# Kernel tuning notes

Measured on AMD Instinct MI355X. Metric: run time of the kernel, lower is better.

The kernel has to match this reference:

```python
import jax, jax.numpy as jnp
import numpy as np

N, E, B, O = 100000, 1600000, 256, 32
D, H, OD = 128, 128, 32  # node_features, hidden_dim, order_encoding_dim
L = 3  # num_layers


def setup_inputs() -> dict:
    key = jax.random.key(0)
    ks = jax.random.split(key, 32)
    g = lambda k, s, fan: jax.random.normal(k, s, jnp.float32) * (1.0 / np.sqrt(fan))
    inp = {
        'x': jax.random.normal(ks[0], (N, D), jnp.float32),
        'edge_index': jax.random.randint(ks[1], (2, E), 0, N),
        'orders': jax.random.normal(ks[2], (B, O, OD), jnp.float32),
        'batch': jnp.sort(jax.random.randint(ks[3], (N,), 0, B)),
        # GIN layers (input_dim == hidden_dim so all 3 layers stack): MLP = Lin(H,H)->ReLU->Lin(H,H), then BatchNorm1d
        'gW1': g(ks[4], (L, H, H), H), 'gb1': jnp.zeros((L, H)),
        'gW2': g(ks[5], (L, H, H), H), 'gb2': jnp.zeros((L, H)),
        'gamma': jnp.ones((L, H)), 'beta': jnp.zeros((L, H)),
        # order encoder: Lin(OD,H)->ReLU->Lin(H,H)
        'oW1': g(ks[6], (OD, H), OD), 'ob1': jnp.zeros((H,)),
        'oW2': g(ks[7], (H, H), H), 'ob2': jnp.zeros((H,)),
        # score head: Lin(4H,H)->ReLU->Lin(H,H//2)->ReLU->Lin(H//2,1)
        'sW1': g(ks[8], (4 * H, H), 4 * H), 'sb1': jnp.zeros((H,)),
        'sW2': g(ks[9], (H, H // 2), H), 'sb2': jnp.zeros((H // 2,)),
        'sW3': g(ks[10], (H // 2, 1), H // 2), 'sb3': jnp.zeros((1,)),
    }
    return inp


def reference(x, edge_index, orders, batch, gW1, gb1, gW2, gb2, gamma, beta,
              oW1, ob1, oW2, ob2, sW1, sb1, sW2, sb2, sW3, sb3):
    n = x.shape[0]
    src, dst = edge_index[0], edge_index[1]
    h = x
    nl = gW1.shape[0]
    for i in range(nl):  # fixed small layer count
        agg = jax.ops.segment_sum(h[src], dst, num_segments=n)  # sum aggregation
        z = agg + h  # (1 + eps) * x with eps = 0 (GINConv default)
        z = jnp.maximum(z @ gW1[i] + gb1[i], 0) @ gW2[i] + gb2[i]
        mu = z.mean(0)
        var = z.var(0)  # biased var, as torch BN uses for normalization
        z = (z - mu) * jax.lax.rsqrt(var + 1e-5) * gamma[i] + beta[i]
        h = jnp.maximum(z, 0) if i < nl - 1 else z  # dropout inactive (eval)
    b = orders.shape[0]
    cnt = jax.ops.segment_sum(jnp.ones((n,), h.dtype), batch, num_segments=b)
    ssum = jax.ops.segment_sum(h, batch, num_segments=b)
    smean = ssum / jnp.maximum(cnt, 1)[:, None]
    smax = jax.ops.segment_max(h, batch, num_segments=b)
    smax = jnp.where(jnp.isfinite(smax), smax, 0)
    graph = jnp.concatenate([smean, smax, ssum], axis=-1)  # [B, 3H]
    # batched over num_orders (equivalent to the python per-order loop)
    oe = jnp.maximum(orders @ oW1 + ob1, 0) @ oW2 + ob2  # [B, O, H]
    comb = jnp.concatenate(
        [jnp.broadcast_to(graph[:, None, :], (b, orders.shape[1], graph.shape[-1])), oe], axis=-1)
    s = jnp.maximum(comb @ sW1 + sb1, 0)
    s = jnp.maximum(s @ sW2 + sb2, 0)
    s = (s @ sW3 + sb3)[..., 0]  # [B, O]
    return s
```

## Files before the change

### kernel.cpp

```cpp
#include <hip/hip_runtime.h>

static constexpr int NN = 100000;
static constexpr int NE = 1600000;
static constexpr int NB = 256;
static constexpr int NO = 32;
static constexpr int HD = 128;
static constexpr long NH = (long)NN * HD;

static constexpr int BSHIFT = 9;
static constexpr int BSIZE = 1 << BSHIFT;
static constexpr int NBUCK = 256;
static constexpr int CHUNK = 16384;
static constexpr int NCHUNK = (NE + CHUNK - 1) / CHUNK;
static constexpr int POOL_ROWS = 64;
static constexpr int POOL_GRID = (NN + POOL_ROWS - 1) / POOL_ROWS;

typedef _Float16 f16x8 __attribute__((ext_vector_type(8)));
typedef _Float16 f16x4 __attribute__((ext_vector_type(4)));
typedef _Float16 f16x2 __attribute__((ext_vector_type(2)));
typedef float f32x4 __attribute__((ext_vector_type(4)));

__device__ __forceinline__ unsigned int encf(float f) {
  unsigned int u = __float_as_uint(f);
  return (u & 0x80000000u) ? ~u : (u | 0x80000000u);
}
__device__ __forceinline__ float decf(unsigned int e) {
  return (e & 0x80000000u) ? __uint_as_float(e & 0x7fffffffu) : __uint_as_float(~e);
}

__global__ void bucket_count(const int* __restrict__ ei, int* __restrict__ bucketTotal) {
  __shared__ int cnt[NBUCK];
  const int t = threadIdx.x;
  cnt[t] = 0;
  __syncthreads();
  long start = (long)blockIdx.x * CHUNK;
  long end = min((long)NE, start + CHUNK);
  for (long e = start + t; e < end; e += 256)
    atomicAdd(&cnt[ei[NE + e] >> BSHIFT], 1);
  __syncthreads();
  if (cnt[t]) atomicAdd(&bucketTotal[t], cnt[t]);
}

__global__ void bucket_scan(const int* __restrict__ bucketTotal, int* __restrict__ bucketBase,
                            int* __restrict__ cursor) {
  __shared__ int part[NBUCK];
  const int t = threadIdx.x;
  int v = bucketTotal[t];
  part[t] = v;
  __syncthreads();
  for (int off = 1; off < NBUCK; off <<= 1) {
    int u = (t >= off) ? part[t - off] : 0;
    __syncthreads();
    part[t] += u;
    __syncthreads();
  }
  int base = part[t] - v;
  bucketBase[t] = base;
  cursor[t] = base;
  if (t == NBUCK - 1) bucketBase[NBUCK] = part[t];
}

__global__ void bucket_scatter(const int* __restrict__ ei, int* __restrict__ cursor,
                               unsigned int* __restrict__ binned) {
  __shared__ int cnt[NBUCK];
  __shared__ int runbase[NBUCK];
  const int t = threadIdx.x;
  cnt[t] = 0;
  __syncthreads();
  long start = (long)blockIdx.x * CHUNK;
  long end = min((long)NE, start + CHUNK);
  for (long e = start + t; e < end; e += 256)
    atomicAdd(&cnt[ei[NE + e] >> BSHIFT], 1);
  __syncthreads();
  int c = cnt[t];
  runbase[t] = c ? atomicAdd(&cursor[t], c) : 0;
  cnt[t] = 0;
  __syncthreads();
  for (long e = start + t; e < end; e += 256) {
    int d = ei[NE + e], s = ei[e];
    int b = d >> BSHIFT;
    int pos = runbase[b] + atomicAdd(&cnt[b], 1);
    binned[pos] = ((unsigned int)s << BSHIFT) | (unsigned int)(d & (BSIZE - 1));
  }
}

__global__ void bucket_csr(const unsigned int* __restrict__ binned,
                           const int* __restrict__ bucketBase,
                           int* __restrict__ rowptr, int* __restrict__ col) {
  __shared__ int cnt[BSIZE];
  __shared__ int excl[BSIZE];
  __shared__ int cur[BSIZE];
  __shared__ int part[256];
  const int b = blockIdx.x;
  const int t = threadIdx.x;
  const int lo = bucketBase[b], hi = bucketBase[b + 1];
  cnt[t] = 0; cnt[t + 256] = 0;
  __syncthreads();
  for (int i = lo + t; i < hi; i += 256)
    atomicAdd(&cnt[binned[i] & (BSIZE - 1)], 1);
  __syncthreads();
  int a0 = cnt[2 * t], a1 = cnt[2 * t + 1];
  int s = a0 + a1;
  part[t] = s;
  __syncthreads();
  for (int off = 1; off < 256; off <<= 1) {
    int u = (t >= off) ? part[t - off] : 0;
    __syncthreads();
    part[t] += u;
    __syncthreads();
  }
  int ebase = part[t] - s;
  excl[2 * t] = ebase;
  excl[2 * t + 1] = ebase + a0;
  __syncthreads();
  const int node0 = b * BSIZE;
  for (int i = t; i < BSIZE; i += 256) {
    int node = node0 + i;
    if (node < NN) rowptr[node] = lo + excl[i] + cnt[i];
    cur[i] = lo + excl[i];
  }
  __syncthreads();
  for (int i = lo + t; i < hi; i += 256) {
    unsigned int v = binned[i];
    int pos = atomicAdd(&cur[v & (BSIZE - 1)], 1);
    col[pos] = (int)(v >> BSHIFT);
  }
}

__global__ void f32to16_kernel(const float* __restrict__ in, _Float16* __restrict__ out) {
  long i = (long)(blockIdx.x * 256 + threadIdx.x) * 8;
  if (i >= NH) return;
  float4 a = *reinterpret_cast<const float4*>(in + i);
  float4 b = *reinterpret_cast<const float4*>(in + i + 4);
  f16x8 v;
  v[0] = (_Float16)a.x; v[1] = (_Float16)a.y; v[2] = (_Float16)a.z; v[3] = (_Float16)a.w;
  v[4] = (_Float16)b.x; v[5] = (_Float16)b.y; v[6] = (_Float16)b.z; v[7] = (_Float16)b.w;
  *reinterpret_cast<f16x8*>(out + i) = v;
}

__global__ void pack_w_kernel(const float* __restrict__ gW1, const float* __restrict__ gW2,
                              _Float16* __restrict__ Wp) {
  int tid = blockIdx.x * blockDim.x + threadIdx.x;
  if (tid >= 12288) return;
  int lane = tid & 63;
  int s = (tid >> 6) & 3;
  int t = (tid >> 8) & 7;
  int which = (tid >> 11) & 1;
  int layer = tid >> 12;
  const float* W = (which ? gW2 : gW1) + (long)layer * 128 * 128;
  _Float16* dst = Wp + (long)tid * 8;
  int kbase = s * 32 + ((lane >> 4) << 3);
  int n = t * 16 + (lane & 15);
#pragma unroll
  for (int j = 0; j < 8; ++j) dst[j] = (_Float16)W[(kbase + j) * 128 + n];
}

__global__ void pack_head_kernel(const float* __restrict__ oW1, const float* __restrict__ oW2,
                                 const float* __restrict__ sW1, const float* __restrict__ sW2,
                                 _Float16* __restrict__ dst) {
  int tid = blockIdx.x * blockDim.x + threadIdx.x;
  if (tid >= 5632) return;
  const float* W; int K, N, rowOff;
  int base = tid;
  if (tid < 512)       { W = oW1; K = 32;  N = 128; rowOff = 0;   }
  else if (tid < 2560) { W = oW2; K = 128; N = 128; rowOff = 0;   base = tid - 512; }
  else if (tid < 4608) { W = sW1; K = 128; N = 128; rowOff = 384; base = tid - 2560; }
  else                 { W = sW2; K = 128; N = 64;  rowOff = 0;   base = tid - 4608; }
  int lane = base & 63;
  int fs = base >> 6;
  int NS = K >> 5;
  int s = fs % NS;
  int tt = fs / NS;
  int k = s * 32 + ((lane >> 4) << 3);
  int n = tt * 16 + (lane & 15);
  _Float16* d = dst + (long)tid * 8;
#pragma unroll
  for (int j = 0; j < 8; ++j) d[j] = (_Float16)W[(long)(rowOff + k + j) * N + n];
}

template <bool BN, bool RELU>
__global__ void gather_kernel(const _Float16* __restrict__ hin, const int* __restrict__ rowptr,
                              const int* __restrict__ col, const float* __restrict__ accum,
                              const float* __restrict__ gamma, const float* __restrict__ beta,
                              _Float16* __restrict__ z) {
  const int node = (blockIdx.x * blockDim.x + threadIdx.x) >> 6;
  if (node >= NN) return;
  const int c2 = (threadIdx.x & 63) * 2;
  float scx = 1.f, scy = 1.f, shx = 0.f, shy = 0.f;
  if (BN) {
    const float n = (float)NN;
    float mu0 = accum[c2] / n, mu1 = accum[c2 + 1] / n;
    float v0 = accum[128 + c2] / n - mu0 * mu0;
    float v1 = accum[128 + c2 + 1] / n - mu1 * mu1;
    scx = rsqrtf(v0 + 1e-5f) * gamma[c2];
    scy = rsqrtf(v1 + 1e-5f) * gamma[c2 + 1];
    shx = beta[c2] - mu0 * scx;
    shy = beta[c2 + 1] - mu1 * scy;
  }
  auto ldh = [&](int n) -> float2 {
    f16x2 h = *reinterpret_cast<const f16x2*>(hin + (long)n * HD + c2);
    float2 v = make_float2((float)h[0], (float)h[1]);
    if (BN) {
      v.x = fmaf(v.x, scx, shx);
      v.y = fmaf(v.y, scy, shy);
      if (RELU) { v.x = fmaxf(v.x, 0.f); v.y = fmaxf(v.y, 0.f); }
    }
    return v;
  };
  const int lo = (node == 0) ? 0 : rowptr[node - 1];
  const int hi = rowptr[node];
  float2 acc = ldh(node);
  int j = lo;
  for (; j + 4 <= hi; j += 4) {
    int s0 = col[j], s1 = col[j + 1], s2 = col[j + 2], s3 = col[j + 3];
    float2 v0 = ldh(s0), v1 = ldh(s1), v2 = ldh(s2), v3 = ldh(s3);
    acc.x += (v0.x + v1.x) + (v2.x + v3.x);
    acc.y += (v0.y + v1.y) + (v2.y + v3.y);
  }
  if (j < hi) {
    int last = hi - 1;
    int s0 = col[j];
    int s1 = col[min(j + 1, last)];
    int s2 = col[min(j + 2, last)];
    int s3 = col[min(j + 3, last)];
    float m1 = (j + 1 < hi) ? 1.f : 0.f;
    float m2 = (j + 2 < hi) ? 1.f : 0.f;
    float m3 = (j + 3 < hi) ? 1.f : 0.f;
    float2 v0 = ldh(s0), v1 = ldh(s1), v2 = ldh(s2), v3 = ldh(s3);
    acc.x += v0.x + m1 * v1.x + m2 * v2.x + m3 * v3.x;
    acc.y += v0.y + m1 * v1.y + m2 * v2.y + m3 * v3.y;
  }
  f16x2 o;
  o[0] = (_Float16)acc.x;
  o[1] = (_Float16)acc.y;
  *reinterpret_cast<f16x2*>(z + (long)node * HD + c2) = o;
}

__global__ void __launch_bounds__(256)
fused_layer(const _Float16* __restrict__ Z, const _Float16* __restrict__ Wp,
            const float* __restrict__ b1, const float* __restrict__ b2,
            _Float16* __restrict__ Z2, float* __restrict__ accum) {
  __shared__ _Float16 Abuf[64 * 136];
  __shared__ _Float16 Hbuf[64 * 136];
  __shared__ float red[256];
  const int t = threadIdx.x;
  const int row0 = blockIdx.x * 64;
  const int lane = t & 63;
  const int w = t >> 6;
  const int l15 = lane & 15;
  const int kgrp = lane >> 4;

  for (int idx = t; idx < 64 * 16; idx += 256) {
    int r = idx >> 4;
    int c8 = (idx & 15) * 8;
    int row = row0 + r;
    f16x8 v = {};
    if (row < NN) v = *reinterpret_cast<const f16x8*>(Z + (long)row * HD + c8);
    *reinterpret_cast<f16x8*>(&Abuf[r * 136 + c8]) = v;
  }
  red[t] = 0.f;
  __syncthreads();

  f32x4 acc[8];
  {
    f16x8 af[4];
#pragma unroll
    for (int s = 0; s < 4; ++s)
      af[s] = *reinterpret_cast<const f16x8*>(&Abuf[(w * 16 + l15) * 136 + s * 32 + kgrp * 8]);
    const _Float16* W1p = Wp;
#pragma unroll
    for (int tt = 0; tt < 8; ++tt) {
      float bb = b1[tt * 16 + l15];
      acc[tt] = (f32x4){bb, bb, bb, bb};
#pragma unroll
      for (int s = 0; s < 4; ++s) {
        f16x8 bf = *reinterpret_cast<const f16x8*>(W1p + ((tt * 4 + s) * 64 + lane) * 8);
        acc[tt] = __builtin_amdgcn_mfma_f32_16x16x32_f16(af[s], bf, acc[tt], 0, 0, 0);
      }
    }
  }
#pragma unroll
  for (int tt = 0; tt < 8; ++tt) {
#pragma unroll
    for (int j = 0; j < 4; ++j) {
      float v = fmaxf(acc[tt][j], 0.f);
      Hbuf[(w * 16 + kgrp * 4 + j) * 136 + tt * 16 + l15] = (_Float16)v;
    }
  }
  {
    f16x8 af[4];
#pragma unroll
    for (int s = 0; s < 4; ++s)
      af[s] = *reinterpret_cast<const f16x8*>(&Hbuf[(w * 16 + l15) * 136 + s * 32 + kgrp * 8]);
    const _Float16* W2p = Wp + 16384;
#pragma unroll
    for (int tt = 0; tt < 8; ++tt) {
      float bb = b2[tt * 16 + l15];
      acc[tt] = (f32x4){bb, bb, bb, bb};
#pragma unroll
      for (int s = 0; s < 4; ++s) {
        f16x8 bf = *reinterpret_cast<const f16x8*>(W2p + ((tt * 4 + s) * 64 + lane) * 8);
        acc[tt] = __builtin_amdgcn_mfma_f32_16x16x32_f16(af[s], bf, acc[tt], 0, 0, 0);
      }
    }
  }
#pragma unroll
  for (int tt = 0; tt < 8; ++tt) {
    int c = tt * 16 + l15;
    float s = 0.f, q = 0.f;
#pragma unroll
    for (int j = 0; j < 4; ++j) {
      int r = row0 + w * 16 + kgrp * 4 + j;
      if (r < NN) {
        float v = acc[tt][j];
        Z2[(long)r * HD + c] = (_Float16)v;
        s += v; q += v * v;
      }
    }
    atomicAdd(&red[c], s);
    atomicAdd(&red[128 + c], q);
  }
  __syncthreads();
  atomicAdd(&accum[t], red[t]);
}

__global__ void pool_init(float* __restrict__ ssum, unsigned int* __restrict__ smaxU) {
  int i = blockIdx.x * 256 + threadIdx.x;
  ssum[i] = 0.f;
  smaxU[i] = 0x007FFFFFu;
}

__global__ void pool_partial(const _Float16* __restrict__ z2, const float* __restrict__ accum,
                             const float* __restrict__ gamma, const float* __restrict__ beta,
                             const int* __restrict__ batch,
                             float* __restrict__ ssum, unsigned int* __restrict__ smaxU) {
  const int c = threadIdx.x;
  const int row0 = blockIdx.x * POOL_ROWS;
  const int rowEnd = min(row0 + POOL_ROWS, NN);
  const float n = (float)NN;
  float mu = accum[c] / n;
  float var = accum[128 + c] / n - mu * mu;
  const float sc = rsqrtf(var + 1e-5f) * gamma[c];
  const float sh = beta[c] - mu * sc;

  int curb = batch[row0];
  float s = 0.f, m = -INFINITY;
  for (int row = row0; row < rowEnd; ++row) {
    int b = batch[row];
    if (b != curb) {
      atomicAdd(&ssum[curb * HD + c], s);
      atomicMax(&smaxU[curb * HD + c], encf(m));
      s = 0.f; m = -INFINITY; curb = b;
    }
    float v = fmaf((float)z2[(long)row * HD + c], sc, sh);
    s += v;
    m = fmaxf(m, v);
  }
  atomicAdd(&ssum[curb * HD + c], s);
  atomicMax(&smaxU[curb * HD + c], encf(m));
}

__global__ void pool_final(const int* __restrict__ batch, float* __restrict__ ssum,
                           unsigned int* __restrict__ smaxU, float* __restrict__ smean,
                           float* __restrict__ smax) {
  const int b = blockIdx.x;
  const int c = threadIdx.x;
  int lo = 0, hi = NN;
  while (lo < hi) { int mid = (lo + hi) >> 1; if (batch[mid] < b) lo = mid + 1; else hi = mid; }
  const int start = lo;
  hi = NN;
  while (lo < hi) { int mid = (lo + hi) >> 1; if (batch[mid] < b + 1) lo = mid + 1; else hi = mid; }
  const int cnt = lo - start;
  float s = ssum[b * HD + c];
  smean[b * HD + c] = s / fmaxf((float)cnt, 1.f);
  smax[b * HD + c] = (cnt > 0) ? decf(smaxU[b * HD + c]) : 0.f;
}

__global__ void gpart_kernel(const float* __restrict__ smean, const float* __restrict__ smax,
                             const float* __restrict__ ssum, const float* __restrict__ sW1,
                             const float* __restrict__ sb1, float* __restrict__ gpart) {
  const int b = blockIdx.x;
  const int j = threadIdx.x;
  float acc = sb1[j];
  for (int k = 0; k < 128; ++k) acc = fmaf(smean[b * HD + k], sW1[k * 128 + j], acc);
  for (int k = 0; k < 128; ++k) acc = fmaf(smax[b * HD + k], sW1[(128 + k) * 128 + j], acc);
  for (int k = 0; k < 128; ++k) acc = fmaf(ssum[b * HD + k], sW1[(256 + k) * 128 + j], acc);
  gpart[b * HD + j] = acc;
}

__global__ void __launch_bounds__(128)
head_mfma(const float* __restrict__ orders, const _Float16* __restrict__ Wh,
          const float* __restrict__ ob1, const float* __restrict__ ob2,
          const float* __restrict__ gpart, const float* __restrict__ sb2,
          const float* __restrict__ sW3, const float* __restrict__ sb3,
          float* __restrict__ out) {
  __shared__ _Float16 B1[32 * 136];
  __shared__ _Float16 B2[32 * 136];
  const int t = threadIdx.x;
  const int g = blockIdx.x;
  const int row0 = g * 32;
  const int lane = t & 63;
  const int w = t >> 6;
  const int l15 = lane & 15;
  const int kgrp = lane >> 4;
  const _Float16* oW1p  = Wh;
  const _Float16* oW2p  = Wh + 4096;
  const _Float16* sW1bp = Wh + 20480;
  const _Float16* sW2p  = Wh + 36864;

  for (int idx = t; idx < 32 * 8; idx += 128) {
    int r = idx >> 3;
    int c4 = (idx & 7) * 4;
    float4 v = *reinterpret_cast<const float4*>(orders + (long)(row0 + r) * 32 + c4);
    f16x4 h;
    h[0] = (_Float16)v.x; h[1] = (_Float16)v.y; h[2] = (_Float16)v.z; h[3] = (_Float16)v.w;
    *reinterpret_cast<f16x4*>(&B1[r * 136 + c4]) = h;
  }
  __syncthreads();

  f32x4 acc[8];
  {
    f16x8 a0 = *reinterpret_cast<const f16x8*>(&B1[(w * 16 + l15) * 136 + kgrp * 8]);
#pragma unroll
    for (int tt = 0; tt < 8; ++tt) {
      float bb = ob1[tt * 16 + l15];
      acc[tt] = (f32x4){bb, bb, bb, bb};
      f16x8 bf = *reinterpret_cast<const f16x8*>(oW1p + (tt * 64 + lane) * 8);
      acc[tt] = __builtin_amdgcn_mfma_f32_16x16x32_f16(a0, bf, acc[tt], 0, 0, 0);
    }
#pragma unroll
    for (int tt = 0; tt < 8; ++tt)
#pragma unroll
      for (int j = 0; j < 4; ++j)
        B2[(w * 16 + kgrp * 4 + j) * 136 + tt * 16 + l15] = (_Float16)fmaxf(acc[tt][j], 0.f);
  }
  {
    f16x8 af[4];
#pragma unroll
    for (int s = 0; s < 4; ++s)
      af[s] = *reinterpret_cast<const f16x8*>(&B2[(w * 16 + l15) * 136 + s * 32 + kgrp * 8]);
#pragma unroll
    for (int tt = 0; tt < 8; ++tt) {
      float bb = ob2[tt * 16 + l15];
      acc[tt] = (f32x4){bb, bb, bb, bb};
#pragma unroll
      for (int s = 0; s < 4; ++s) {
        f16x8 bf = *reinterpret_cast<const f16x8*>(oW2p + ((tt * 4 + s) * 64 + lane) * 8);
        acc[tt] = __builtin_amdgcn_mfma_f32_16x16x32_f16(af[s], bf, acc[tt], 0, 0, 0);
      }
    }
#pragma unroll
    for (int tt = 0; tt < 8; ++tt)
#pragma unroll
      for (int j = 0; j < 4; ++j)
        B1[(w * 16 + kgrp * 4 + j) * 136 + tt * 16 + l15] = (_Float16)acc[tt][j];
  }
  {
    f16x8 af[4];
#pragma unroll
    for (int s = 0; s < 4; ++s)
      af[s] = *reinterpret_cast<const f16x8*>(&B1[(w * 16 + l15) * 136 + s * 32 + kgrp * 8]);
#pragma unroll
    for (int tt = 0; tt < 8; ++tt) {
      acc[tt] = (f32x4){0.f, 0.f, 0.f, 0.f};
#pragma unroll
      for (int s = 0; s < 4; ++s) {
        f16x8 bf = *reinterpret_cast<const f16x8*>(sW1bp + ((tt * 4 + s) * 64 + lane) * 8);
        acc[tt] = __builtin_amdgcn_mfma_f32_16x16x32_f16(af[s], bf, acc[tt], 0, 0, 0);
      }
    }
#pragma unroll
    for (int tt = 0; tt < 8; ++tt) {
      int c = tt * 16 + l15;
      float gp = gpart[g * HD + c];
#pragma unroll
      for (int j = 0; j < 4; ++j)
        B2[(w * 16 + kgrp * 4 + j) * 136 + c] = (_Float16)fmaxf(acc[tt][j] + gp, 0.f);
    }
  }
  {
    f16x8 af[4];
#pragma unroll
    for (int s = 0; s < 4; ++s)
      af[s] = *reinterpret_cast<const f16x8*>(&B2[(w * 16 + l15) * 136 + s * 32 + kgrp * 8]);
#pragma unroll
    for (int tt = 0; tt < 4; ++tt) {
      float bb = sb2[tt * 16 + l15];
      acc[tt] = (f32x4){bb, bb, bb, bb};
#pragma unroll
      for (int s = 0; s < 4; ++s) {
        f16x8 bf = *reinterpret_cast<const f16x8*>(sW2p + ((tt * 4 + s) * 64 + lane) * 8);
        acc[tt] = __builtin_amdgcn_mfma_f32_16x16x32_f16(af[s], bf, acc[tt], 0, 0, 0);
      }
    }
    float rsum[4] = {0.f, 0.f, 0.f, 0.f};
#pragma unroll
    for (int tt = 0; tt < 4; ++tt) {
      float wv = sW3[tt * 16 + l15];
#pragma unroll
      for (int j = 0; j < 4; ++j)
        rsum[j] = fmaf(fmaxf(acc[tt][j], 0.f), wv, rsum[j]);
    }
#pragma unroll
    for (int j = 0; j < 4; ++j) {
      rsum[j] += __shfl_xor(rsum[j], 1);
      rsum[j] += __shfl_xor(rsum[j], 2);
      rsum[j] += __shfl_xor(rsum[j], 4);
      rsum[j] += __shfl_xor(rsum[j], 8);
    }
    if (l15 == 0) {
      float b3 = sb3[0];
#pragma unroll
      for (int j = 0; j < 4; ++j)
        out[row0 + w * 16 + kgrp * 4 + j] = rsum[j] + b3;
    }
  }
}

extern "C" void kernel_launch(void* const* d_in, const int* in_sizes, int n_in,
                              void* d_out, int out_size, void* d_ws, size_t ws_size,
                              hipStream_t stream) {
  const float* x      = (const float*)d_in[0];
  const int*   ei     = (const int*)d_in[1];
  const float* orders = (const float*)d_in[2];
  const int*   batch  = (const int*)d_in[3];
  const float* gW1    = (const float*)d_in[4];
  const float* gb1    = (const float*)d_in[5];
  const float* gW2    = (const float*)d_in[6];
  const float* gb2    = (const float*)d_in[7];
  const float* gamma  = (const float*)d_in[8];
  const float* beta   = (const float*)d_in[9];
  const float* oW1    = (const float*)d_in[10];
  const float* ob1    = (const float*)d_in[11];
  const float* oW2    = (const float*)d_in[12];
  const float* ob2    = (const float*)d_in[13];
  const float* sW1    = (const float*)d_in[14];
  const float* sb1    = (const float*)d_in[15];
  const float* sW2    = (const float*)d_in[16];
  const float* sb2    = (const float*)d_in[17];
  const float* sW3    = (const float*)d_in[18];
  const float* sb3    = (const float*)d_in[19];
  float* out = (float*)d_out;

  char* ws = (char*)d_ws;
  _Float16* xh    = (_Float16*)ws;
  _Float16* bufAh = xh + NH;
  _Float16* bufCh = bufAh + NH;
  float* accum = (float*)(bufCh + NH);
  float* ssum  = accum + 256;
  float* smean = ssum + NB * HD;
  float* smax  = smean + NB * HD;
  unsigned int* smaxU = (unsigned int*)(smax + NB * HD);
  float* gpart = (float*)(smaxU + NB * HD);
  int* rowptr = (int*)(gpart + NB * HD);
  int* col    = rowptr + NN;
  unsigned int* binned = (unsigned int*)(col + NE);
  int* bucketTotal = (int*)(binned + NE);
  int* bucketBase  = bucketTotal + NBUCK;
  int* cursor      = bucketBase + NBUCK + 1;
  _Float16* Wp  = (_Float16*)(cursor + NBUCK);
  _Float16* Wh  = Wp + 3 * 32768;

  hipMemsetAsync(bucketTotal, 0, NBUCK * sizeof(int), stream);
  bucket_count<<<NCHUNK, 256, 0, stream>>>(ei, bucketTotal);
  bucket_scan<<<1, NBUCK, 0, stream>>>(bucketTotal, bucketBase, cursor);
  bucket_scatter<<<NCHUNK, 256, 0, stream>>>(ei, cursor, binned);
  bucket_csr<<<NBUCK, 256, 0, stream>>>(binned, bucketBase, rowptr, col);

  pack_w_kernel<<<48, 256, 0, stream>>>(gW1, gW2, Wp);
  pack_head_kernel<<<22, 256, 0, stream>>>(oW1, oW2, sW1, sW2, Wh);
  f32to16_kernel<<<(int)(NH / 8 + 255) / 256, 256, 0, stream>>>(x, xh);

  const int GATHER_GRID = NN / 4;
  const int LAYER_GRID = (NN + 63) / 64;
  for (int l = 0; l < 3; ++l) {
    if (l == 0)
      gather_kernel<false, false><<<GATHER_GRID, 256, 0, stream>>>(
          xh, rowptr, col, accum, gamma, beta, bufAh);
    else
      gather_kernel<true, true><<<GATHER_GRID, 256, 0, stream>>>(
          bufCh, rowptr, col, accum, gamma + (l - 1) * 128, beta + (l - 1) * 128, bufAh);
    hipMemsetAsync(accum, 0, 256 * sizeof(float), stream);
    fused_layer<<<LAYER_GRID, 256, 0, stream>>>(
        bufAh, Wp + (long)l * 32768, gb1 + l * 128, gb2 + l * 128, bufCh, accum);
  }

  pool_init<<<128, 256, 0, stream>>>(ssum, smaxU);
  pool_partial<<<POOL_GRID, 128, 0, stream>>>(bufCh, accum, gamma + 2 * 128, beta + 2 * 128,
                                              batch, ssum, smaxU);
  pool_final<<<NB, 128, 0, stream>>>(batch, ssum, smaxU, smean, smax);

  gpart_kernel<<<NB, 128, 0, stream>>>(smean, smax, ssum, sW1, sb1, gpart);
  head_mfma<<<NB, 128, 0, stream>>>(orders, Wh, ob1, ob2, gpart, sb2, sW3, sb3, out);
}
```

Baseline: 596.6 us.

## Fuse neighbor gather into GIN MLP kernel and shard BN stat atomics

Merges the CSR sum-aggregation into the fused MLP kernel, so each block aggregates its 64 nodes straight into shared memory instead of writing and rereading an intermediate fp16 buffer. The hidden buffer now reuses the same LDS array. BatchNorm statistic atomics are spread over 64 sub-accumulators and summed by a small reduce kernel, which cuts global atomic contention. The gather now runs with only 4 waves per 64 nodes, each wave walking 16 nodes one after another, so memory-level parallelism per CU may drop compared with the separate gather launch.

```diff
diff --git a/kernel.cpp b/kernel.cpp
--- a/kernel.cpp
+++ b/kernel.cpp
@@ -14,6 +14,7 @@
 static constexpr int NCHUNK = (NE + CHUNK - 1) / CHUNK;
 static constexpr int POOL_ROWS = 64;
 static constexpr int POOL_GRID = (NN + POOL_ROWS - 1) / POOL_ROWS;
+static constexpr int NSUB = 64;
 
 typedef _Float16 f16x8 __attribute__((ext_vector_type(8)));
 typedef _Float16 f16x4 __attribute__((ext_vector_type(4)));
@@ -178,70 +179,15 @@
   for (int j = 0; j < 8; ++j) d[j] = (_Float16)W[(long)(rowOff + k + j) * N + n];
 }
 
-template <bool BN, bool RELU>
-__global__ void gather_kernel(const _Float16* __restrict__ hin, const int* __restrict__ rowptr,
-                              const int* __restrict__ col, const float* __restrict__ accum,
-                              const float* __restrict__ gamma, const float* __restrict__ beta,
-                              _Float16* __restrict__ z) {
-  const int node = (blockIdx.x * blockDim.x + threadIdx.x) >> 6;
-  if (node >= NN) return;
-  const int c2 = (threadIdx.x & 63) * 2;
-  float scx = 1.f, scy = 1.f, shx = 0.f, shy = 0.f;
-  if (BN) {
-    const float n = (float)NN;
-    float mu0 = accum[c2] / n, mu1 = accum[c2 + 1] / n;
-    float v0 = accum[128 + c2] / n - mu0 * mu0;
-    float v1 = accum[128 + c2 + 1] / n - mu1 * mu1;
-    scx = rsqrtf(v0 + 1e-5f) * gamma[c2];
-    scy = rsqrtf(v1 + 1e-5f) * gamma[c2 + 1];
-    shx = beta[c2] - mu0 * scx;
-    shy = beta[c2 + 1] - mu1 * scy;
-  }
-  auto ldh = [&](int n) -> float2 {
-    f16x2 h = *reinterpret_cast<const f16x2*>(hin + (long)n * HD + c2);
-    float2 v = make_float2((float)h[0], (float)h[1]);
-    if (BN) {
-      v.x = fmaf(v.x, scx, shx);
-      v.y = fmaf(v.y, scy, shy);
-      if (RELU) { v.x = fmaxf(v.x, 0.f); v.y = fmaxf(v.y, 0.f); }
-    }
-    return v;
-  };
-  const int lo = (node == 0) ? 0 : rowptr[node - 1];
-  const int hi = rowptr[node];
-  float2 acc = ldh(node);
-  int j = lo;
-  for (; j + 4 <= hi; j += 4) {
-    int s0 = col[j], s1 = col[j + 1], s2 = col[j + 2], s3 = col[j + 3];
-    float2 v0 = ldh(s0), v1 = ldh(s1), v2 = ldh(s2), v3 = ldh(s3);
-    acc.x += (v0.x + v1.x) + (v2.x + v3.x);
-    acc.y += (v0.y + v1.y) + (v2.y + v3.y);
-  }
-  if (j < hi) {
-    int last = hi - 1;
-    int s0 = col[j];
-    int s1 = col[min(j + 1, last)];
-    int s2 = col[min(j + 2, last)];
-    int s3 = col[min(j + 3, last)];
-    float m1 = (j + 1 < hi) ? 1.f : 0.f;
-    float m2 = (j + 2 < hi) ? 1.f : 0.f;
-    float m3 = (j + 3 < hi) ? 1.f : 0.f;
-    float2 v0 = ldh(s0), v1 = ldh(s1), v2 = ldh(s2), v3 = ldh(s3);
-    acc.x += v0.x + m1 * v1.x + m2 * v2.x + m3 * v3.x;
-    acc.y += v0.y + m1 * v1.y + m2 * v2.y + m3 * v3.y;
-  }
-  f16x2 o;
-  o[0] = (_Float16)acc.x;
-  o[1] = (_Float16)acc.y;
-  *reinterpret_cast<f16x2*>(z + (long)node * HD + c2) = o;
-}
-
+template <bool BN>
 __global__ void __launch_bounds__(256)
-fused_layer(const _Float16* __restrict__ Z, const _Float16* __restrict__ Wp,
-            const float* __restrict__ b1, const float* __restrict__ b2,
-            _Float16* __restrict__ Z2, float* __restrict__ accum) {
+fused_gin(const _Float16* __restrict__ Hprev, const int* __restrict__ rowptr,
+          const int* __restrict__ col, const float* __restrict__ accum,
+          const float* __restrict__ gamma, const float* __restrict__ beta,
+          const _Float16* __restrict__ Wp,
+          const float* __restrict__ b1, const float* __restrict__ b2,
+          _Float16* __restrict__ Z2, float* __restrict__ accum2) {
   __shared__ _Float16 Abuf[64 * 136];
-  __shared__ _Float16 Hbuf[64 * 136];
   __shared__ float red[256];
   const int t = threadIdx.x;
   const int row0 = blockIdx.x * 64;
@@ -249,16 +195,66 @@
   const int w = t >> 6;
   const int l15 = lane & 15;
   const int kgrp = lane >> 4;
-
-  for (int idx = t; idx < 64 * 16; idx += 256) {
-    int r = idx >> 4;
-    int c8 = (idx & 15) * 8;
-    int row = row0 + r;
-    f16x8 v = {};
-    if (row < NN) v = *reinterpret_cast<const f16x8*>(Z + (long)row * HD + c8);
-    *reinterpret_cast<f16x8*>(&Abuf[r * 136 + c8]) = v;
-  }
   red[t] = 0.f;
+
+  {
+    const int c2 = lane * 2;
+    float scx = 1.f, scy = 1.f, shx = 0.f, shy = 0.f;
+    if (BN) {
+      const float n = (float)NN;
+      float mu0 = accum[c2] / n, mu1 = accum[c2 + 1] / n;
+      float v0 = accum[128 + c2] / n - mu0 * mu0;
+      float v1 = accum[128 + c2 + 1] / n - mu1 * mu1;
+      scx = rsqrtf(v0 + 1e-5f) * gamma[c2];
+      scy = rsqrtf(v1 + 1e-5f) * gamma[c2 + 1];
+      shx = beta[c2] - mu0 * scx;
+      shy = beta[c2 + 1] - mu1 * scy;
+    }
+    auto ldh = [&](int n) -> float2 {
+      f16x2 h = *reinterpret_cast<const f16x2*>(Hprev + (long)n * HD + c2);
+      float2 v = make_float2((float)h[0], (float)h[1]);
+      if (BN) {
+        v.x = fmaxf(fmaf(v.x, scx, shx), 0.f);
+        v.y = fmaxf(fmaf(v.y, scy, shy), 0.f);
+      }
+      return v;
+    };
+    for (int i = 0; i < 16; ++i) {
+      const int nodeRow = w * 16 + i;
+      const int node = row0 + nodeRow;
+      float ax = 0.f, ay = 0.f;
+      if (node < NN) {
+        const int lo = (node == 0) ? 0 : rowptr[node - 1];
+        const int hi = rowptr[node];
+        float2 a = ldh(node);
+        ax = a.x; ay = a.y;
+        int j = lo;
+        for (; j + 4 <= hi; j += 4) {
+          int s0 = col[j], s1 = col[j + 1], s2 = col[j + 2], s3 = col[j + 3];
+          float2 v0 = ldh(s0), v1 = ldh(s1), v2 = ldh(s2), v3 = ldh(s3);
+          ax += (v0.x + v1.x) + (v2.x + v3.x);
+          ay += (v0.y + v1.y) + (v2.y + v3.y);
+        }
+        if (j < hi) {
+          int last = hi - 1;
+          int s0 = col[j];
+          int s1 = col[min(j + 1, last)];
+          int s2 = col[min(j + 2, last)];
+          int s3 = col[min(j + 3, last)];
+          float m1 = (j + 1 < hi) ? 1.f : 0.f;
+          float m2 = (j + 2 < hi) ? 1.f : 0.f;
+          float m3 = (j + 3 < hi) ? 1.f : 0.f;
+          float2 v0 = ldh(s0), v1 = ldh(s1), v2 = ldh(s2), v3 = ldh(s3);
+          ax += v0.x + m1 * v1.x + m2 * v2.x + m3 * v3.x;
+          ay += v0.y + m1 * v1.y + m2 * v2.y + m3 * v3.y;
+        }
+      }
+      f16x2 o;
+      o[0] = (_Float16)ax;
+      o[1] = (_Float16)ay;
+      *reinterpret_cast<f16x2*>(&Abuf[nodeRow * 136 + c2]) = o;
+    }
+  }
   __syncthreads();
 
   f32x4 acc[8];
@@ -284,14 +280,14 @@
 #pragma unroll
     for (int j = 0; j < 4; ++j) {
       float v = fmaxf(acc[tt][j], 0.f);
-      Hbuf[(w * 16 + kgrp * 4 + j) * 136 + tt * 16 + l15] = (_Float16)v;
+      Abuf[(w * 16 + kgrp * 4 + j) * 136 + tt * 16 + l15] = (_Float16)v;
     }
   }
   {
     f16x8 af[4];
 #pragma unroll
     for (int s = 0; s < 4; ++s)
-      af[s] = *reinterpret_cast<const f16x8*>(&Hbuf[(w * 16 + l15) * 136 + s * 32 + kgrp * 8]);
+      af[s] = *reinterpret_cast<const f16x8*>(&Abuf[(w * 16 + l15) * 136 + s * 32 + kgrp * 8]);
     const _Float16* W2p = Wp + 16384;
 #pragma unroll
     for (int tt = 0; tt < 8; ++tt) {
@@ -321,7 +317,14 @@
     atomicAdd(&red[128 + c], q);
   }
   __syncthreads();
-  atomicAdd(&accum[t], red[t]);
+  atomicAdd(&accum2[(blockIdx.x & (NSUB - 1)) * 256 + t], red[t]);
+}
+
+__global__ void bn_reduce(const float* __restrict__ accum2, float* __restrict__ accum) {
+  const int c = threadIdx.x;
+  float s = 0.f;
+  for (int i = 0; i < NSUB; ++i) s += accum2[i * 256 + c];
+  accum[c] = s;
 }
 
 __global__ void pool_init(float* __restrict__ ssum, unsigned int* __restrict__ smaxU) {
@@ -546,10 +549,11 @@
   _Float16* xh    = (_Float16*)ws;
   _Float16* bufAh = xh + NH;
   _Float16* bufCh = bufAh + NH;
-  float* accum = (float*)(bufCh + NH);
-  float* ssum  = accum + 256;
-  float* smean = ssum + NB * HD;
-  float* smax  = smean + NB * HD;
+  float* accum  = (float*)(bufCh + NH);
+  float* accum2 = accum + 256;
+  float* ssum   = accum2 + NSUB * 256;
+  float* smean  = ssum + NB * HD;
+  float* smax   = smean + NB * HD;
   unsigned int* smaxU = (unsigned int*)(smax + NB * HD);
   float* gpart = (float*)(smaxU + NB * HD);
   int* rowptr = (int*)(gpart + NB * HD);
@@ -571,18 +575,20 @@
   pack_head_kernel<<<22, 256, 0, stream>>>(oW1, oW2, sW1, sW2, Wh);
   f32to16_kernel<<<(int)(NH / 8 + 255) / 256, 256, 0, stream>>>(x, xh);
 
-  const int GATHER_GRID = NN / 4;
   const int LAYER_GRID = (NN + 63) / 64;
+  const _Float16* src[3] = {xh, bufCh, bufAh};
+  _Float16* dst[3] = {bufCh, bufAh, bufCh};
   for (int l = 0; l < 3; ++l) {
+    hipMemsetAsync(accum2, 0, NSUB * 256 * sizeof(float), stream);
     if (l == 0)
-      gather_kernel<false, false><<<GATHER_GRID, 256, 0, stream>>>(
-          xh, rowptr, col, accum, gamma, beta, bufAh);
+      fused_gin<false><<<LAYER_GRID, 256, 0, stream>>>(
+          src[l], rowptr, col, accum, gamma, beta, Wp,
+          gb1, gb2, dst[l], accum2);
     else
-      gather_kernel<true, true><<<GATHER_GRID, 256, 0, stream>>>(
-          bufCh, rowptr, col, accum, gamma + (l - 1) * 128, beta + (l - 1) * 128, bufAh);
-    hipMemsetAsync(accum, 0, 256 * sizeof(float), stream);
-    fused_layer<<<LAYER_GRID, 256, 0, stream>>>(
-        bufAh, Wp + (long)l * 32768, gb1 + l * 128, gb2 + l * 128, bufCh, accum);
+      fused_gin<true><<<LAYER_GRID, 256, 0, stream>>>(
+          src[l], rowptr, col, accum, gamma + (l - 1) * 128, beta + (l - 1) * 128,
+          Wp + (long)l * 32768, gb1 + l * 128, gb2 + l * 128, dst[l], accum2);
+    bn_reduce<<<1, 256, 0, stream>>>(accum2, accum);
   }
 
   pool_init<<<128, 256, 0, stream>>>(ssum, smaxU);
```

After: 793.8 us. 33.1% more time.
